# Kernel optimization log

Hardware: AMD Instinct MI355X
Metric: run time of the kernel (lower is better)

The kernel has to match this reference:

```python
import jax, jax.numpy as jnp
import numpy as np

B, T, E, H = 4, 2048, 1024, 16
S = E // H

def setup_inputs() -> dict:
    key = jax.random.key(0)
    ks = jax.random.split(key, 4)
    x = jax.random.normal(ks[0], (B, T, E), dtype=jnp.float32)
    Wk = jax.random.normal(ks[1], (E, E), dtype=jnp.float32) * (E ** -0.5)
    Wq = jax.random.normal(ks[2], (E, E), dtype=jnp.float32) * (E ** -0.5)
    Wo = jax.random.normal(ks[3], (E, E), dtype=jnp.float32) * (E ** -0.5)
    bo = jnp.zeros((E,), dtype=jnp.float32)
    return {"x": x, "Wk": Wk, "Wq": Wq, "Wo": Wo, "bo": bo}

def reference(x, Wk, Wq, Wo, bo):
    b, t, e = x.shape
    h, s = H, E // H
    scale = e ** (-0.25)  # original scales q and k each by e**(1/4)
    k = (x @ Wk).reshape(b, t, h, s).transpose(0, 2, 1, 3)  # bhts
    q = (x @ Wq).reshape(b, t, h, s).transpose(0, 2, 1, 3)
    # FAITHFUL to source: values use the KEYS projection (bug in original)
    v = (x @ Wk).reshape(b, t, h, s).transpose(0, 2, 1, 3)
    dot = jnp.einsum('bhqd,bhkd->bhqk', q * scale, k * scale)
    attn = jax.nn.softmax(dot, axis=-1)
    out = jnp.einsum('bhqk,bhkd->bhqd', attn, v)
    out = out.transpose(0, 2, 1, 3).reshape(b, t, e)
    return out @ Wo + bo
```

## Files before the change

kernel.cpp:

```cpp
#include <hip/hip_runtime.h>
#include <hip/hip_bf16.h>
#include <stdint.h>

static constexpr int kB = 4;
static constexpr int kT = 2048;
static constexpr int kE = 1024;
static constexpr int kH = 16;
static constexpr int kS = 64;
static constexpr int kRows = kB * kT;

typedef __attribute__((ext_vector_type(4)))  float    f32x4;
typedef __attribute__((ext_vector_type(16))) float    f32x16;
typedef __attribute__((ext_vector_type(4)))  float    float4v;
typedef __attribute__((ext_vector_type(8)))  __bf16   bf16x8;
typedef __attribute__((ext_vector_type(8)))  short    short8v;
typedef __attribute__((ext_vector_type(4)))  short    short4v;
typedef __attribute__((ext_vector_type(2)))  unsigned u32x2;
typedef __attribute__((ext_vector_type(4)))  unsigned u32x4;

typedef const __attribute__((address_space(1))) void gvoid_t;
typedef __attribute__((address_space(3))) void lvoid_t;

__device__ __forceinline__ short f2bf(float f) {
  union { float f; unsigned u; } c; c.f = f;
  unsigned r = (c.u + 0x7FFFu + ((c.u >> 16) & 1u)) >> 16;
  return (short)(r & 0xFFFFu);
}

__device__ __forceinline__ short bfc(float f) {
  union { __bf16 b; short s; } u; u.b = (__bf16)f; return u.s;
}

__device__ __forceinline__ unsigned cvt_pk(float lo, float hi) {
  unsigned r;
  asm("v_cvt_pk_bf16_f32 %0, %1, %2" : "=v"(r) : "v"(lo), "v"(hi));
  return r;
}

__device__ __forceinline__ void plane_swap(unsigned& a, unsigned& b) {
  asm("v_permlane32_swap_b32 %0, %1" : "+v"(a), "+v"(b));
}

#if __has_builtin(__builtin_amdgcn_exp2f)
__device__ __forceinline__ float fexp2(float x) { return __builtin_amdgcn_exp2f(x); }
#else
__device__ __forceinline__ float fexp2(float x) { return exp2f(x); }
#endif

__global__ __launch_bounds__(256)
void prep(const float* __restrict__ x, const float* __restrict__ Wk,
          const float* __restrict__ Wq, const float* __restrict__ Wo,
          short* __restrict__ Xb, short* __restrict__ WkqT,
          short* __restrict__ WoT) {
  const int bid = blockIdx.x;
  if (bid < 8192) {
    size_t i = ((size_t)bid * 256 + threadIdx.x) * 4;
    float4v v = *(const float4v*)(x + i);
    short4v o;
    o[0] = f2bf(v[0]); o[1] = f2bf(v[1]); o[2] = f2bf(v[2]); o[3] = f2bf(v[3]);
    *(short4v*)(Xb + i) = o;
    return;
  }
  __shared__ float tile[32][33];
  const int tb = bid - 8192;
  const int which = tb >> 10, t = tb & 1023;
  const float* W = (which == 0) ? Wk : ((which == 1) ? Wq : Wo);
  short* WT = (which == 0) ? WkqT : ((which == 1) ? (WkqT + kE * kE) : WoT);
  const int tx = threadIdx.x & 31, ty = threadIdx.x >> 5;
  const int c = (t & 31) * 32, r = (t >> 5) * 32;
  #pragma unroll
  for (int i = ty; i < 32; i += 8)
    tile[i][tx] = W[(size_t)(r + i) * kE + c + tx];
  __syncthreads();
  #pragma unroll
  for (int i = ty; i < 32; i += 8)
    WT[(size_t)(c + i) * kE + r + tx] = f2bf(tile[tx][i]);
}


__device__ __forceinline__ void kq_stageA(
    const short* __restrict__ gA, short* nA, int wid, int sl, int sc7) {
  #pragma unroll
  for (int h = 0; h < 2; ++h)
    #pragma unroll
    for (int i = 0; i < 2; ++i) {
      const int slot = wid * 2 + i;
      const int row = slot * 8 + sl;
      const int sc = sc7 ^ (row & 7);
      __builtin_amdgcn_global_load_lds(
          (gvoid_t*)(gA + (size_t)(h * 128 + row) * kE + 8 * sc),
          (lvoid_t*)(nA + h * 8192 + slot * 512), 16, 0, 0);
    }
}

__device__ __forceinline__ void bt_stageB(
    const short* __restrict__ gB, short* nB, int wid, int sl, int sc7) {
  #pragma unroll
  for (int i = 0; i < 2; ++i) {
    const int slot = wid * 2 + i;
    const int row = slot * 8 + sl;
    const int sc = sc7 ^ (row & 7);
    __builtin_amdgcn_global_load_lds(
        (gvoid_t*)(gB + (size_t)row * kE + 8 * sc),
        (lvoid_t*)(nB + slot * 512), 16, 0, 0);
  }
}

__device__ __forceinline__ void kq_tile(
    const short* __restrict__ gA, const short* __restrict__ gB,
    const short* cA, const short* cB, short* nA, short* nB,
    bool stage, f32x4 (&acc)[8][4],
    int wid, int wm, int wn, int g, int lr, int sl, int sc7) {
  const int swz = lr & 7;
  const short* cAw = cA + wm * 8192;
  const short* cBw = cB + (wn >> 1) * 8192;
  const int brow0 = (wn & 1) * 64;
  bf16x8 af[4][2], b0[2][2], b1[2][2];

  #pragma unroll
  for (int mf = 0; mf < 4; ++mf)
    #pragma unroll
    for (int kk = 0; kk < 2; ++kk)
      af[mf][kk] = *(const bf16x8*)(cAw + (mf * 16 + lr) * 64 + (((4 * kk + g) ^ swz) << 3));
  #pragma unroll
  for (int nf = 0; nf < 2; ++nf)
    #pragma unroll
    for (int kk = 0; kk < 2; ++kk)
      b0[nf][kk] = *(const bf16x8*)(cBw + (brow0 + nf * 16 + lr) * 64 + (((4 * kk + g) ^ swz) << 3));
  if (stage) kq_stageA(gA, nA, wid, sl, sc7);
  asm volatile("" ::: "memory");
  __builtin_amdgcn_s_barrier();
  asm volatile("s_waitcnt lgkmcnt(0)" ::: "memory");
  __builtin_amdgcn_sched_barrier(0);
  __builtin_amdgcn_s_setprio(1);
  #pragma unroll
  for (int mf = 0; mf < 4; ++mf)
    #pragma unroll
    for (int nf = 0; nf < 2; ++nf)
      #pragma unroll
      for (int kk = 0; kk < 2; ++kk)
        acc[mf][nf] = __builtin_amdgcn_mfma_f32_16x16x32_bf16(af[mf][kk], b0[nf][kk], acc[mf][nf], 0, 0, 0);
  __builtin_amdgcn_s_setprio(0);
  asm volatile("" ::: "memory");
  __builtin_amdgcn_s_barrier();

  #pragma unroll
  for (int nf = 0; nf < 2; ++nf)
    #pragma unroll
    for (int kk = 0; kk < 2; ++kk)
      b1[nf][kk] = *(const bf16x8*)(cBw + (brow0 + 32 + nf * 16 + lr) * 64 + (((4 * kk + g) ^ swz) << 3));
  if (stage) kq_stageA(gB, nB, wid, sl, sc7);
  asm volatile("" ::: "memory");
  __builtin_amdgcn_s_barrier();
  asm volatile("s_waitcnt lgkmcnt(0)" ::: "memory");
  __builtin_amdgcn_sched_barrier(0);
  __builtin_amdgcn_s_setprio(1);
  #pragma unroll
  for (int mf = 0; mf < 4; ++mf)
    #pragma unroll
    for (int nf = 0; nf < 2; ++nf)
      #pragma unroll
      for (int kk = 0; kk < 2; ++kk)
        acc[mf][2 + nf] = __builtin_amdgcn_mfma_f32_16x16x32_bf16(af[mf][kk], b1[nf][kk], acc[mf][2 + nf], 0, 0, 0);
  __builtin_amdgcn_s_setprio(0);
  asm volatile("" ::: "memory");
  __builtin_amdgcn_s_barrier();

  #pragma unroll
  for (int mf = 0; mf < 4; ++mf)
    #pragma unroll
    for (int kk = 0; kk < 2; ++kk)
      af[mf][kk] = *(const bf16x8*)(cAw + (64 + mf * 16 + lr) * 64 + (((4 * kk + g) ^ swz) << 3));
  asm volatile("" ::: "memory");
  __builtin_amdgcn_s_barrier();
  asm volatile("s_waitcnt lgkmcnt(0)" ::: "memory");
  __builtin_amdgcn_sched_barrier(0);
  __builtin_amdgcn_s_setprio(1);
  #pragma unroll
  for (int mf = 0; mf < 4; ++mf)
    #pragma unroll
    for (int nf = 0; nf < 2; ++nf)
      #pragma unroll
      for (int kk = 0; kk < 2; ++kk)
        acc[4 + mf][2 + nf] = __builtin_amdgcn_mfma_f32_16x16x32_bf16(af[mf][kk], b1[nf][kk], acc[4 + mf][2 + nf], 0, 0, 0);
  __builtin_amdgcn_s_setprio(0);
  asm volatile("" ::: "memory");
  __builtin_amdgcn_s_barrier();

  #pragma unroll
  for (int nf = 0; nf < 2; ++nf)
    #pragma unroll
    for (int kk = 0; kk < 2; ++kk)
      b0[nf][kk] = *(const bf16x8*)(cBw + (brow0 + nf * 16 + lr) * 64 + (((4 * kk + g) ^ swz) << 3));
  asm volatile("s_waitcnt vmcnt(0)" ::: "memory");
  asm volatile("" ::: "memory");
  __builtin_amdgcn_s_barrier();
  asm volatile("s_waitcnt lgkmcnt(0)" ::: "memory");
  __builtin_amdgcn_sched_barrier(0);
  __builtin_amdgcn_s_setprio(1);
  #pragma unroll
  for (int mf = 0; mf < 4; ++mf)
    #pragma unroll
    for (int nf = 0; nf < 2; ++nf)
      #pragma unroll
      for (int kk = 0; kk < 2; ++kk)
        acc[4 + mf][nf] = __builtin_amdgcn_mfma_f32_16x16x32_bf16(af[mf][kk], b0[nf][kk], acc[4 + mf][nf], 0, 0, 0);
  __builtin_amdgcn_s_setprio(0);
  asm volatile("" ::: "memory");
  __builtin_amdgcn_s_barrier();
}

__global__ __launch_bounds__(512)
void gemm_kq8(const short* __restrict__ A, const short* __restrict__ BT,
              short* __restrict__ Kb, short* __restrict__ Qb,
              short* __restrict__ KT, float qs) {
  __shared__ short LA[2][16384];
  __shared__ short LB[2][16384];

  const int tid = threadIdx.x;
  const int wid = tid >> 6, lane = tid & 63;
  const int g = lane >> 4, lr = lane & 15;
  const int wm = wid >> 2, wn = wid & 3;
  const int sl = lane >> 3, sc7 = lane & 7;
  const int bid = blockIdx.x;
  const int id = (bid & 7) * 32 + (bid >> 3);
  const int n0 = (id & 7) * 256, m0 = (id >> 3) * 256;

  const short* Abase = A + (size_t)m0 * kE;
  const short* Bbase = BT + (size_t)n0 * kE;

  f32x4 acc[8][4];
  #pragma unroll
  for (int mf = 0; mf < 8; ++mf)
    #pragma unroll
    for (int nf = 0; nf < 4; ++nf)
      #pragma unroll
      for (int r = 0; r < 4; ++r) acc[mf][nf][r] = 0.f;

  kq_stageA(Abase, &LA[0][0], wid, sl, sc7);
  kq_stageA(Bbase, &LB[0][0], wid, sl, sc7);
  asm volatile("s_waitcnt vmcnt(0)" ::: "memory");
  __syncthreads();

  for (int ktp = 0; ktp < 8; ++ktp) {
    kq_tile(Abase + (2 * ktp + 1) * 64, Bbase + (2 * ktp + 1) * 64,
            &LA[0][0], &LB[0][0], &LA[1][0], &LB[1][0],
            true, acc, wid, wm, wn, g, lr, sl, sc7);
    kq_tile(Abase + (2 * ktp + 2) * 64, Bbase + (2 * ktp + 2) * 64,
            &LA[1][0], &LB[1][0], &LA[0][0], &LB[0][0],
            (2 * ktp + 1) < 15, acc, wid, wm, wn, g, lr, sl, sc7);
  }

  const int isq = (n0 >= 1024);
  short* Crm = isq ? Qb : Kb;
  const float scale = isq ? qs : 1.0f;
  const int crow = m0 + wm * 128, ccol = (n0 & 1023) + wn * 64;
  #pragma unroll
  for (int mf = 0; mf < 8; ++mf)
    #pragma unroll
    for (int nf = 0; nf < 4; ++nf)
      #pragma unroll
      for (int r = 0; r < 4; ++r)
        Crm[(size_t)(crow + mf * 16 + 4 * g + r) * kE + ccol + nf * 16 + lr] =
            bfc(acc[mf][nf][r] * scale);
  if (!isq) {
    const int b = m0 >> 11, tloc = (m0 & 2047) + wm * 128;
    const int h = (n0 + wn * 64) >> 6;
    #pragma unroll
    for (int mf = 0; mf < 8; ++mf)
      #pragma unroll
      for (int nf = 0; nf < 4; ++nf) {
        u32x2 e;
        e[0] = cvt_pk(acc[mf][nf][0], acc[mf][nf][1]);
        e[1] = cvt_pk(acc[mf][nf][2], acc[mf][nf][3]);
        *(u32x2*)(KT + (size_t)((b * 16 + h) * 64 + nf * 16 + lr) * kT +
                  tloc + mf * 16 + 4 * g) = e;
      }
  }
}

__global__ __launch_bounds__(512)
void gemm_bt8(const short* __restrict__ A, const short* __restrict__ BT,
              float* __restrict__ C, const float* __restrict__ bias) {
  __shared__ short LA[2][16384];
  __shared__ short LB[2][8192];

  const int tid = threadIdx.x;
  const int wid = tid >> 6, lane = tid & 63;
  const int g = lane >> 4, lr = lane & 15;
  const int wm = wid >> 1, wn = wid & 1;
  const int sl = lane >> 3, sc7 = lane & 7;
  const int swz = lr & 7;
  const int bid = blockIdx.x;
  const int id = (bid & 7) * 32 + (bid >> 3);
  const int n0 = (id & 7) * 128, m0 = (id >> 3) * 256;

  const short* Abase = A + (size_t)m0 * kE;
  const short* Bbase = BT + (size_t)n0 * kE;

  f32x4 acc[4][4];
  #pragma unroll
  for (int mf = 0; mf < 4; ++mf)
    #pragma unroll
    for (int nf = 0; nf < 4; ++nf)
      #pragma unroll
      for (int r = 0; r < 4; ++r) acc[mf][nf][r] = 0.f;

  kq_stageA(Abase, &LA[0][0], wid, sl, sc7);
  bt_stageB(Bbase, &LB[0][0], wid, sl, sc7);
  asm volatile("s_waitcnt vmcnt(0)" ::: "memory");
  __syncthreads();

  for (int ktp = 0; ktp < 8; ++ktp) {
    #pragma unroll
    for (int half = 0; half < 2; ++half) {
      const int kt = 2 * ktp + half;
      const short* cA = &LA[kt & 1][0];
      const short* cB = &LB[kt & 1][0];
      short* nA = &LA[(kt + 1) & 1][0];
      short* nB = &LB[(kt + 1) & 1][0];
      const bool stage = kt < 15;
      const short* gA = Abase + (kt + 1) * 64;
      const short* gB = Bbase + (kt + 1) * 64;
      const short* cAw = cA + wm * 4096;
      const short* cBw = cB + wn * 4096;
      bf16x8 af[2][2], b0[2][2], b1[2][2];

      #pragma unroll
      for (int mf = 0; mf < 2; ++mf)
        #pragma unroll
        for (int kk = 0; kk < 2; ++kk)
          af[mf][kk] = *(const bf16x8*)(cAw + (mf * 16 + lr) * 64 + (((4 * kk + g) ^ swz) << 3));
      #pragma unroll
      for (int nf = 0; nf < 2; ++nf)
        #pragma unroll
        for (int kk = 0; kk < 2; ++kk)
          b0[nf][kk] = *(const bf16x8*)(cBw + (nf * 16 + lr) * 64 + (((4 * kk + g) ^ swz) << 3));
      if (stage) kq_stageA(gA, nA, wid, sl, sc7);
      asm volatile("" ::: "memory");
      __builtin_amdgcn_s_barrier();
      asm volatile("s_waitcnt lgkmcnt(0)" ::: "memory");
      __builtin_amdgcn_sched_barrier(0);
      __builtin_amdgcn_s_setprio(1);
      #pragma unroll
      for (int mf = 0; mf < 2; ++mf)
        #pragma unroll
        for (int nf = 0; nf < 2; ++nf)
          #pragma unroll
          for (int kk = 0; kk < 2; ++kk)
            acc[mf][nf] = __builtin_amdgcn_mfma_f32_16x16x32_bf16(af[mf][kk], b0[nf][kk], acc[mf][nf], 0, 0, 0);
      __builtin_amdgcn_s_setprio(0);
      asm volatile("" ::: "memory");
      __builtin_amdgcn_s_barrier();

      #pragma unroll
      for (int nf = 0; nf < 2; ++nf)
        #pragma unroll
        for (int kk = 0; kk < 2; ++kk)
          b1[nf][kk] = *(const bf16x8*)(cBw + (32 + nf * 16 + lr) * 64 + (((4 * kk + g) ^ swz) << 3));
      if (stage) bt_stageB(gB, nB, wid, sl, sc7);
      asm volatile("" ::: "memory");
      __builtin_amdgcn_s_barrier();
      asm volatile("s_waitcnt lgkmcnt(0)" ::: "memory");
      __builtin_amdgcn_sched_barrier(0);
      __builtin_amdgcn_s_setprio(1);
      #pragma unroll
      for (int mf = 0; mf < 2; ++mf)
        #pragma unroll
        for (int nf = 0; nf < 2; ++nf)
          #pragma unroll
          for (int kk = 0; kk < 2; ++kk)
            acc[mf][2 + nf] = __builtin_amdgcn_mfma_f32_16x16x32_bf16(af[mf][kk], b1[nf][kk], acc[mf][2 + nf], 0, 0, 0);
      __builtin_amdgcn_s_setprio(0);
      asm volatile("" ::: "memory");
      __builtin_amdgcn_s_barrier();

      #pragma unroll
      for (int mf = 0; mf < 2; ++mf)
        #pragma unroll
        for (int kk = 0; kk < 2; ++kk)
          af[mf][kk] = *(const bf16x8*)(cAw + (32 + mf * 16 + lr) * 64 + (((4 * kk + g) ^ swz) << 3));
      asm volatile("" ::: "memory");
      __builtin_amdgcn_s_barrier();
      asm volatile("s_waitcnt lgkmcnt(0)" ::: "memory");
      __builtin_amdgcn_sched_barrier(0);
      __builtin_amdgcn_s_setprio(1);
      #pragma unroll
      for (int mf = 0; mf < 2; ++mf)
        #pragma unroll
        for (int nf = 0; nf < 2; ++nf)
          #pragma unroll
          for (int kk = 0; kk < 2; ++kk)
            acc[2 + mf][2 + nf] = __builtin_amdgcn_mfma_f32_16x16x32_bf16(af[mf][kk], b1[nf][kk], acc[2 + mf][2 + nf], 0, 0, 0);
      __builtin_amdgcn_s_setprio(0);
      asm volatile("" ::: "memory");
      __builtin_amdgcn_s_barrier();

      asm volatile("s_waitcnt vmcnt(0)" ::: "memory");
      asm volatile("" ::: "memory");
      __builtin_amdgcn_s_barrier();
      __builtin_amdgcn_sched_barrier(0);
      __builtin_amdgcn_s_setprio(1);
      #pragma unroll
      for (int mf = 0; mf < 2; ++mf)
        #pragma unroll
        for (int nf = 0; nf < 2; ++nf)
          #pragma unroll
          for (int kk = 0; kk < 2; ++kk)
            acc[2 + mf][nf] = __builtin_amdgcn_mfma_f32_16x16x32_bf16(af[mf][kk], b0[nf][kk], acc[2 + mf][nf], 0, 0, 0);
      __builtin_amdgcn_s_setprio(0);
      asm volatile("" ::: "memory");
      __builtin_amdgcn_s_barrier();
    }
  }

  const int crow = m0 + wm * 64, ccol = n0 + wn * 64;
  float bv[4];
  #pragma unroll
  for (int nf = 0; nf < 4; ++nf) bv[nf] = bias[ccol + nf * 16 + lr];
  #pragma unroll
  for (int mf = 0; mf < 4; ++mf)
    #pragma unroll
    for (int nf = 0; nf < 4; ++nf)
      #pragma unroll
      for (int r = 0; r < 4; ++r)
        C[(size_t)(crow + mf * 16 + 4 * g + r) * kE + ccol + nf * 16 + lr] =
            acc[mf][nf][r] + bv[nf];
}

__global__ __launch_bounds__(256, 4)
void attn_kernel(const short* Qb, const short* __restrict__ Kb,
                 const short* __restrict__ KT, short* AO) {
  __shared__ short SM[16384];

  const int tid = threadIdx.x;
  const int w = tid >> 6, lane = tid & 63;
  const int l31 = lane & 31, hi = lane >> 5;
  const int swz = l31 & 7;
  const int bid = blockIdx.x;
  const int id = (bid & 7) * 128 + (bid >> 3);
  const int q0 = (id & 15) * 128;
  const int bh = id >> 4;
  const size_t base = (size_t)(bh >> 4) * kT * kE + (size_t)(bh & 15) * kS;
  const short* Kbh = Kb + base;
  const short* KTbh = KT + (size_t)bh * 64 * kT;

  const int srow_lo = lane >> 3, sch = lane & 7;

  #pragma unroll
  for (int i = 0; i < 2; ++i) {
    const int slot = w * 2 + i, row = slot * 8 + srow_lo;
    const int sc = sch ^ (row & 7);
    __builtin_amdgcn_global_load_lds(
        (gvoid_t*)(Kbh + (size_t)row * kE + 8 * sc),
        (lvoid_t*)(SM + slot * 512), 16, 0, 0);
    __builtin_amdgcn_global_load_lds(
        (gvoid_t*)(KTbh + (size_t)row * kT + 8 * sc),
        (lvoid_t*)(SM + 8192 + slot * 512), 16, 0, 0);
  }

  bf16x8 qB[4];
  #pragma unroll
  for (int ks = 0; ks < 4; ++ks)
    qB[ks] = *(const bf16x8*)(Qb + base +
        (size_t)(q0 + w * 32 + l31) * kE + ks * 16 + hi * 8);

  f32x16 oacc[2];
  #pragma unroll
  for (int r = 0; r < 16; ++r) { oacc[0][r] = 0.f; oacc[1][r] = 0.f; }
  float lsum = 0.f;

  for (int t = 0; t < 32; ++t) {
    __syncthreads();

    if (t < 31) {
      const short* kbt = Kbh + (size_t)(t + 1) * 64 * kE;
      const short* vtt = KTbh + (size_t)(t + 1) * 64;
      short* KtN = SM + ((t + 1) & 1) * 4096;
      short* VtN = SM + 8192 + ((t + 1) & 1) * 4096;
      #pragma unroll
      for (int i = 0; i < 2; ++i) {
        const int slot = w * 2 + i, row = slot * 8 + srow_lo;
        const int sc = sch ^ (row & 7);
        __builtin_amdgcn_global_load_lds(
            (gvoid_t*)(kbt + (size_t)row * kE + 8 * sc),
            (lvoid_t*)(KtN + slot * 512), 16, 0, 0);
        __builtin_amdgcn_global_load_lds(
            (gvoid_t*)(vtt + (size_t)row * kT + 8 * sc),
            (lvoid_t*)(VtN + slot * 512), 16, 0, 0);
      }
    }

    const short* KtC = SM + (t & 1) * 4096;
    const short* VtC = SM + 8192 + (t & 1) * 4096;

    f32x16 sacc[2];
    #pragma unroll
    for (int r = 0; r < 16; ++r) { sacc[0][r] = 0.f; sacc[1][r] = 0.f; }
    #pragma unroll
    for (int ks = 0; ks < 4; ++ks) {
      const int pc = ((2 * ks + hi) ^ swz) << 3;
      bf16x8 kf0 = *(const bf16x8*)(KtC + (l31)      * 64 + pc);
      bf16x8 kf1 = *(const bf16x8*)(KtC + (32 + l31) * 64 + pc);
      __builtin_amdgcn_s_setprio(1);
      sacc[0] = __builtin_amdgcn_mfma_f32_32x32x16_bf16(kf0, qB[ks], sacc[0], 0, 0, 0);
      sacc[1] = __builtin_amdgcn_mfma_f32_32x32x16_bf16(kf1, qB[ks], sacc[1], 0, 0, 0);
      __builtin_amdgcn_s_setprio(0);
    }

    union { unsigned u[4]; bf16x8 v; } pf[4];
    #pragma unroll
    for (int kvf = 0; kvf < 2; ++kvf) {
      float pe[16];
      #pragma unroll
      for (int r = 0; r < 16; ++r) {
        pe[r] = fexp2(sacc[kvf][r]);
        lsum += pe[r];
      }
      #pragma unroll
      for (int sub = 0; sub < 2; ++sub) {
        unsigned a0 = cvt_pk(pe[8 * sub + 0], pe[8 * sub + 1]);
        unsigned b0 = cvt_pk(pe[8 * sub + 4], pe[8 * sub + 5]);
        plane_swap(a0, b0);
        unsigned a1 = cvt_pk(pe[8 * sub + 2], pe[8 * sub + 3]);
        unsigned b1 = cvt_pk(pe[8 * sub + 6], pe[8 * sub + 7]);
        plane_swap(a1, b1);
        pf[2 * kvf + sub].u[0] = a0;
        pf[2 * kvf + sub].u[1] = a1;
        pf[2 * kvf + sub].u[2] = b0;
        pf[2 * kvf + sub].u[3] = b1;
      }
    }

    #pragma unroll
    for (int ks = 0; ks < 4; ++ks) {
      const int pc = ((2 * ks + hi) ^ swz) << 3;
      bf16x8 vf0 = *(const bf16x8*)(VtC + (l31)      * 64 + pc);
      bf16x8 vf1 = *(const bf16x8*)(VtC + (32 + l31) * 64 + pc);
      __builtin_amdgcn_s_setprio(1);
      oacc[0] = __builtin_amdgcn_mfma_f32_32x32x16_bf16(vf0, pf[ks].v, oacc[0], 0, 0, 0);
      oacc[1] = __builtin_amdgcn_mfma_f32_32x32x16_bf16(vf1, pf[ks].v, oacc[1], 0, 0, 0);
      __builtin_amdgcn_s_setprio(0);
    }
  }

  __syncthreads();

  const float ltot = lsum + __shfl_xor(lsum, 32);
  const float inv = 1.f / ltot;
  short* OtW = SM + w * 2176;
  #pragma unroll
  for (int sf = 0; sf < 2; ++sf)
    #pragma unroll
    for (int c = 0; c < 4; ++c) {
      u32x2 e;
      e[0] = cvt_pk(oacc[sf][4 * c + 0] * inv, oacc[sf][4 * c + 1] * inv);
      e[1] = cvt_pk(oacc[sf][4 * c + 2] * inv, oacc[sf][4 * c + 3] * inv);
      *(u32x2*)(OtW + l31 * 68 + sf * 32 + 8 * c + 4 * hi) = e;
    }
  __builtin_amdgcn_s_barrier();
  #pragma unroll
  for (int i = 0; i < 8; ++i) {
    const int row = i * 4 + (lane >> 4);
    u32x2 v = *(const u32x2*)(OtW + row * 68 + (lane & 15) * 4);
    *(u32x2*)(AO + base + (size_t)(q0 + w * 32 + row) * kE + (lane & 15) * 4) = v;
  }
}

extern "C" void kernel_launch(void* const* d_in, const int* in_sizes, int n_in,
                              void* d_out, int out_size, void* d_ws, size_t ws_size,
                              hipStream_t stream) {
  const float* x  = (const float*)d_in[0];
  const float* Wk = (const float*)d_in[1];
  const float* Wq = (const float*)d_in[2];
  const float* Wo = (const float*)d_in[3];
  const float* bo = (const float*)d_in[4];
  float* out = (float*)d_out;

  const size_t nXE = (size_t)kRows * kE;
  const size_t nW  = (size_t)kE * kE;

  short* Xb   = (short*)d_ws;
  short* Kb   = Xb   + nXE;
  short* Qb   = Kb   + nXE;
  short* WkqT = Qb   + nXE;
  short* WoT  = WkqT + 2 * nW;
  short* KTb  = (short*)d_out;
  short* AO   = Qb;

  prep<<<dim3(8192 + 3 * 1024), 256, 0, stream>>>(
      x, Wk, Wq, Wo, Xb, WkqT, WoT);

  gemm_kq8<<<dim3(256), 512, 0, stream>>>(
      Xb, WkqT, Kb, Qb, KTb, 0.03125f * 1.44269504f);

  attn_kernel<<<dim3(1024), 256, 0, stream>>>(Qb, Kb, KTb, AO);

  gemm_bt8<<<dim3(256), 512, 0, stream>>>(AO, WoT, out, bo);
}
```

Baseline: 160.7 us.

## Double attention query tile to 256 rows with 8 waves per block

The attention kernel now runs 512 threads (8 waves) per block over 256 query rows, with half as many blocks. Each K/V tile staged in LDS is therefore shared by twice as many waves, which halves the global K/V traffic and the per-wave load issue count. The output epilogue is split into two rounds so the existing LDS staging buffer can be reused by 4 waves at a time. The trade-offs are fewer blocks (512) to fill the CUs, the launch_bounds occupancy hint is dropped, and each barrier now synchronises 8 waves.

```diff
diff --git a/kernel.cpp b/kernel.cpp
--- a/kernel.cpp
+++ b/kernel.cpp
@@ -428,7 +428,7 @@
             acc[mf][nf][r] + bv[nf];
 }
 
-__global__ __launch_bounds__(256, 4)
+__global__ __launch_bounds__(512)
 void attn_kernel(const short* Qb, const short* __restrict__ Kb,
                  const short* __restrict__ KT, short* AO) {
   __shared__ short SM[16384];
@@ -438,26 +438,24 @@
   const int l31 = lane & 31, hi = lane >> 5;
   const int swz = l31 & 7;
   const int bid = blockIdx.x;
-  const int id = (bid & 7) * 128 + (bid >> 3);
-  const int q0 = (id & 15) * 128;
-  const int bh = id >> 4;
+  const int id = (bid & 7) * 64 + (bid >> 3);
+  const int q0 = (id & 7) * 256;
+  const int bh = id >> 3;
   const size_t base = (size_t)(bh >> 4) * kT * kE + (size_t)(bh & 15) * kS;
   const short* Kbh = Kb + base;
   const short* KTbh = KT + (size_t)bh * 64 * kT;
 
   const int srow_lo = lane >> 3, sch = lane & 7;
-
-  #pragma unroll
-  for (int i = 0; i < 2; ++i) {
-    const int slot = w * 2 + i, row = slot * 8 + srow_lo;
-    const int sc = sch ^ (row & 7);
-    __builtin_amdgcn_global_load_lds(
-        (gvoid_t*)(Kbh + (size_t)row * kE + 8 * sc),
-        (lvoid_t*)(SM + slot * 512), 16, 0, 0);
-    __builtin_amdgcn_global_load_lds(
-        (gvoid_t*)(KTbh + (size_t)row * kT + 8 * sc),
-        (lvoid_t*)(SM + 8192 + slot * 512), 16, 0, 0);
-  }
+  const int srow = w * 8 + srow_lo;
+  const int ssc = sch ^ (srow & 7);
+  const size_t koff = (size_t)srow * kE + 8 * ssc;
+  const size_t voff = (size_t)srow * kT + 8 * ssc;
+  const int sdst = w * 512;
+
+  __builtin_amdgcn_global_load_lds((gvoid_t*)(Kbh + koff),
+                                   (lvoid_t*)(SM + sdst), 16, 0, 0);
+  __builtin_amdgcn_global_load_lds((gvoid_t*)(KTbh + voff),
+                                   (lvoid_t*)(SM + 8192 + sdst), 16, 0, 0);
 
   bf16x8 qB[4];
   #pragma unroll
@@ -478,17 +476,10 @@
       const short* vtt = KTbh + (size_t)(t + 1) * 64;
       short* KtN = SM + ((t + 1) & 1) * 4096;
       short* VtN = SM + 8192 + ((t + 1) & 1) * 4096;
-      #pragma unroll
-      for (int i = 0; i < 2; ++i) {
-        const int slot = w * 2 + i, row = slot * 8 + srow_lo;
-        const int sc = sch ^ (row & 7);
-        __builtin_amdgcn_global_load_lds(
-            (gvoid_t*)(kbt + (size_t)row * kE + 8 * sc),
-            (lvoid_t*)(KtN + slot * 512), 16, 0, 0);
-        __builtin_amdgcn_global_load_lds(
-            (gvoid_t*)(vtt + (size_t)row * kT + 8 * sc),
-            (lvoid_t*)(VtN + slot * 512), 16, 0, 0);
-      }
+      __builtin_amdgcn_global_load_lds((gvoid_t*)(kbt + koff),
+                                       (lvoid_t*)(KtN + sdst), 16, 0, 0);
+      __builtin_amdgcn_global_load_lds((gvoid_t*)(vtt + voff),
+                                       (lvoid_t*)(VtN + sdst), 16, 0, 0);
     }
 
     const short* KtC = SM + (t & 1) * 4096;
@@ -544,26 +535,29 @@
     }
   }
 
-  __syncthreads();
-
   const float ltot = lsum + __shfl_xor(lsum, 32);
   const float inv = 1.f / ltot;
-  short* OtW = SM + w * 2176;
-  #pragma unroll
-  for (int sf = 0; sf < 2; ++sf)
-    #pragma unroll
-    for (int c = 0; c < 4; ++c) {
-      u32x2 e;
-      e[0] = cvt_pk(oacc[sf][4 * c + 0] * inv, oacc[sf][4 * c + 1] * inv);
-      e[1] = cvt_pk(oacc[sf][4 * c + 2] * inv, oacc[sf][4 * c + 3] * inv);
-      *(u32x2*)(OtW + l31 * 68 + sf * 32 + 8 * c + 4 * hi) = e;
-    }
-  __builtin_amdgcn_s_barrier();
-  #pragma unroll
-  for (int i = 0; i < 8; ++i) {
-    const int row = i * 4 + (lane >> 4);
-    u32x2 v = *(const u32x2*)(OtW + row * 68 + (lane & 15) * 4);
-    *(u32x2*)(AO + base + (size_t)(q0 + w * 32 + row) * kE + (lane & 15) * 4) = v;
+  short* OtW = SM + (w & 3) * 2176;
+  #pragma unroll
+  for (int round = 0; round < 2; ++round) {
+    __syncthreads();
+    if ((w >> 2) == round) {
+      #pragma unroll
+      for (int sf = 0; sf < 2; ++sf)
+        #pragma unroll
+        for (int c = 0; c < 4; ++c) {
+          u32x2 e;
+          e[0] = cvt_pk(oacc[sf][4 * c + 0] * inv, oacc[sf][4 * c + 1] * inv);
+          e[1] = cvt_pk(oacc[sf][4 * c + 2] * inv, oacc[sf][4 * c + 3] * inv);
+          *(u32x2*)(OtW + l31 * 68 + sf * 32 + 8 * c + 4 * hi) = e;
+        }
+      #pragma unroll
+      for (int i = 0; i < 8; ++i) {
+        const int row = i * 4 + (lane >> 4);
+        u32x2 v = *(const u32x2*)(OtW + row * 68 + (lane & 15) * 4);
+        *(u32x2*)(AO + base + (size_t)(q0 + w * 32 + row) * kE + (lane & 15) * 4) = v;
+      }
+    }
   }
 }
 
@@ -594,7 +588,7 @@
   gemm_kq8<<<dim3(256), 512, 0, stream>>>(
       Xb, WkqT, Kb, Qb, KTb, 0.03125f * 1.44269504f);
 
-  attn_kernel<<<dim3(1024), 256, 0, stream>>>(Qb, Kb, KTb, AO);
+  attn_kernel<<<dim3(512), 512, 0, stream>>>(Qb, Kb, KTb, AO);
 
   gemm_bt8<<<dim3(256), 512, 0, stream>>>(AO, WoT, out, bo);
 }
```

Result: faster. 153.7 us (-4.3%).
